# Kernel optimization log

Measured on AMD Instinct MI355X. Metric: run time of the kernel, lower is better.

The kernel has to match this reference:

```python
import jax, jax.numpy as jnp
import numpy as np

N_HEAD = 12

def setup_inputs() -> dict:
    key = jax.random.key(0)
    k1, k2, k3, k4, k5 = jax.random.split(key, 5)
    B, T, C = 2, 2048, 768
    x = jax.random.normal(k1, (B, T, C), dtype=jnp.float32)
    W_attn = jax.random.normal(k2, (C, 3 * C), dtype=jnp.float32) * 0.02
    b_attn = jax.random.normal(k3, (3 * C,), dtype=jnp.float32) * 0.02
    W_proj = jax.random.normal(k4, (C, C), dtype=jnp.float32) * 0.02
    b_proj = jax.random.normal(k5, (C,), dtype=jnp.float32) * 0.02
    return {"x": x, "W_attn": W_attn, "b_attn": b_attn, "W_proj": W_proj, "b_proj": b_proj}

def reference(x, W_attn, b_attn, W_proj, b_proj):
    B, T, C = x.shape
    H = N_HEAD
    hd = C // H
    qkv = x @ W_attn + b_attn  # [B,T,3C]
    q, k, v = jnp.split(qkv, 3, axis=2)
    # [B,H,T,hd]
    q = q.reshape(B, T, H, hd).transpose(0, 2, 1, 3)
    k = k.reshape(B, T, H, hd).transpose(0, 2, 1, 3)
    v = v.reshape(B, T, H, hd).transpose(0, 2, 1, 3)
    att = jnp.einsum('bhqd,bhkd->bhqk', q, k) / jnp.sqrt(jnp.float32(hd))
    causal = jnp.tril(jnp.ones((T, T), dtype=bool))
    att = jnp.where(causal[None, None], att, -jnp.inf)
    att = jax.nn.softmax(att, axis=-1)
    y = jnp.einsum('bhqk,bhkd->bhqd', att, v)  # [B,H,T,hd]
    y = y.transpose(0, 2, 1, 3).reshape(B, T, C)
    return y @ W_proj + b_proj
```

## Files before the change

kernel.cpp:

```cpp
#include <hip/hip_runtime.h>
#include <stdint.h>

typedef unsigned short u16;
typedef __attribute__((ext_vector_type(8))) short bf16x8;
typedef __attribute__((ext_vector_type(4))) float f32x4;

__device__ __forceinline__ u16 f2bf(float f){
  union { float f; uint32_t u; } v; v.f = f;
  uint32_t u = v.u;
  u += 0x7FFFu + ((u >> 16) & 1u);
  return (u16)(u >> 16);
}

__device__ __forceinline__ float fexp2(float x){
#if __has_builtin(__builtin_amdgcn_exp2f)
  return __builtin_amdgcn_exp2f(x);
#else
  return exp2f(x);
#endif
}

__device__ __forceinline__ uint32_t cvtpk_bf16(float lo, float hi){
  uint32_t d;
  asm("v_cvt_pk_bf16_f32 %0, %1, %2" : "=v"(d) : "v"(lo), "v"(hi));
  return d;
}

__device__ __forceinline__ f32x4 mfma_bf16(bf16x8 a, bf16x8 b, f32x4 c){
  return __builtin_amdgcn_mfma_f32_16x16x32_bf16(a, b, c, 0, 0, 0);
}

#define QSCALE 0.1803368801111244f

__global__ __launch_bounds__(256) void cast_x_k(const float* __restrict__ x,
                                                u16* __restrict__ xb, int n4){
  int i = blockIdx.x*256 + threadIdx.x;
  if (i >= n4) return;
  float4 v = reinterpret_cast<const float4*>(x)[i];
  uint2 o;
  o.x = (uint32_t)f2bf(v.x) | ((uint32_t)f2bf(v.y) << 16);
  o.y = (uint32_t)f2bf(v.z) | ((uint32_t)f2bf(v.w) << 16);
  reinterpret_cast<uint2*>(xb)[i] = o;
}

__global__ __launch_bounds__(256) void transpose_cast_k(const float* __restrict__ in,
                                                        u16* __restrict__ out,
                                                        int R, int C){
  __shared__ u16 tile[64][66];
  int c0 = blockIdx.x*64, r0 = blockIdx.y*64;
  int tc = threadIdx.x & 63, t4 = threadIdx.x >> 6;
  #pragma unroll
  for (int i=0;i<16;i++){ int r = t4 + i*4; tile[r][tc] = f2bf(in[(size_t)(r0+r)*C + c0 + tc]); }
  __syncthreads();
  #pragma unroll
  for (int i=0;i<16;i++){ int cc = t4 + i*4; out[(size_t)(c0+cc)*R + r0 + tc] = tile[tc][cc]; }
}

#define LDP 40

__global__ __launch_bounds__(256) void gemm_bf16_k(
    const u16* __restrict__ A, const u16* __restrict__ Bt,
    int M, int N, int K, const float* __restrict__ bias, int mode,
    u16* __restrict__ qo, u16* __restrict__ ko, u16* __restrict__ vo,
    float* __restrict__ fo)
{
  __shared__ u16 As[128*LDP];
  __shared__ u16 Bs[128*LDP];
  const int m0 = blockIdx.y*128, n0 = blockIdx.x*128;
  const int tid = threadIdx.x, lane = tid & 63, wid = tid >> 6;
  const int lr = lane & 15, lg = lane >> 4;
  const int wr = wid >> 1, wc = wid & 1;
  f32x4 acc[4][4] = {};
  const int nk = K >> 5;
  for (int kk = 0; kk < nk; ++kk){
    #pragma unroll
    for (int s = 0; s < 2; ++s){
      int ci = tid + 256*s;
      int row = ci >> 2, ch = ci & 3;
      *(uint4*)&As[row*LDP + ch*8] = *(const uint4*)&A[(size_t)(m0+row)*K + kk*32 + ch*8];
      *(uint4*)&Bs[row*LDP + ch*8] = *(const uint4*)&Bt[(size_t)(n0+row)*K + kk*32 + ch*8];
    }
    __syncthreads();
    bf16x8 af[4], bfr[4];
    #pragma unroll
    for (int m=0;m<4;m++) af[m] = *(const bf16x8*)&As[(wr*64 + m*16 + lr)*LDP + lg*8];
    #pragma unroll
    for (int n=0;n<4;n++) bfr[n] = *(const bf16x8*)&Bs[(wc*64 + n*16 + lr)*LDP + lg*8];
    #pragma unroll
    for (int m=0;m<4;m++)
      #pragma unroll
      for (int n=0;n<4;n++)
        acc[m][n] = mfma_bf16(af[m], bfr[n], acc[m][n]);
    __syncthreads();
  }
  if (mode == 0){
    #pragma unroll
    for (int m=0;m<4;m++)
      #pragma unroll
      for (int n=0;n<4;n++){
        int gn = n0 + wc*64 + n*16 + lr;
        float bv = bias[gn];
        #pragma unroll
        for (int r=0;r<4;r++){
          int gm = m0 + wr*64 + m*16 + lg*4 + r;
          fo[(size_t)gm*N + gn] = acc[m][n][r] + bv;
        }
      }
  } else {
    int which = n0 / 768;
    u16* dst = (which==0) ? qo : ko;
    float sc = (which==0) ? QSCALE : 1.0f;
    #pragma unroll
    for (int m=0;m<4;m++)
      #pragma unroll
      for (int n=0;n<4;n++){
        int gn = n0 + wc*64 + n*16 + lr;
        float bv = bias[gn];
        int cn = gn - which*768;
        int h = cn >> 6, d = cn & 63;
        int gm0 = m0 + wr*64 + m*16 + lg*4;
        int b = gm0 >> 11, t0 = gm0 & 2047;
        if (which < 2){
          #pragma unroll
          for (int r=0;r<4;r++)
            dst[(size_t)((b*12 + h)*2048 + t0 + r)*64 + d] = f2bf((acc[m][n][r] + bv)*sc);
        } else {
          uint2 o;
          o.x = cvtpk_bf16(acc[m][n][0]+bv, acc[m][n][1]+bv);
          o.y = cvtpk_bf16(acc[m][n][2]+bv, acc[m][n][3]+bv);
          *(uint2*)&vo[((size_t)((b*12 + h)*64 + d))*2048 + t0] = o;
        }
      }
  }
}

__global__ __launch_bounds__(256) void attn_k(
    const u16* __restrict__ qp, const u16* __restrict__ kp,
    const u16* __restrict__ vtp, u16* __restrict__ yp)
{
  __shared__ f32x4 ylh[16][64];
  __shared__ float llh[4][16];
  const int i = blockIdx.x;
  const int bh = i % 24;
  const int qb = 63 - (i / 24);
  const int q0 = qb * 32;
  const int q0A = q0, q0B = q0 + 16;
  const int b = bh / 12, h = bh - b*12;
  const size_t base = (size_t)bh * 131072;
  const int tid = threadIdx.x, lane = tid & 63, wid = tid >> 6;
  const int lr = lane & 15, lg = lane >> 4;
  const int qgA = q0A + lr, qgB = q0B + lr;
  const u16* kbase = kp + base;
  const u16* vbase = vtp + base;

  bf16x8 qfA[2], qfB[2];
  #pragma unroll
  for (int kb=0;kb<2;kb++){
    qfA[kb] = *(const bf16x8*)&qp[base + (size_t)qgA*64 + kb*32 + lg*8];
    qfB[kb] = *(const bf16x8*)&qp[base + (size_t)qgB*64 + kb*32 + lg*8];
  }

  f32x4 yA[4] = {}, yB[4] = {};
  float lA = 0.f, lB = 0.f;
  const float m2 = 8.f;
  const int nt = (qb >> 1) + 1;

  uint32_t ko[8], vo[8];
  #pragma unroll
  for (int nb=0;nb<4;nb++){
    int ke = ((nb&1)*32 + (lr>>2)*8 + (nb>>1)*4 + (lr&3))*64 + lg*8;
    ko[nb*2+0] = (uint32_t)(wid*4096 + ke) * 2u;
    ko[nb*2+1] = (uint32_t)(wid*4096 + ke + 32) * 2u;
  }
  #pragma unroll
  for (int n=0;n<4;n++){
    int ve = (n*16+lr)*2048 + lg*8 + wid*64;
    vo[n*2+0] = (uint32_t)ve * 2u;
    vo[n*2+1] = (uint32_t)(ve + 32) * 2u;
  }

  for (int t = wid; t < nt; t += 4){
    bf16x8 kf[8], vf[8];
    #pragma unroll
    for (int j=0;j<8;j++) kf[j] = *(const bf16x8*)((const char*)kbase + ko[j]);
    #pragma unroll
    for (int j=0;j<8;j++) vf[j] = *(const bf16x8*)((const char*)vbase + vo[j]);
    #pragma unroll
    for (int j=0;j<8;j++){ ko[j] += 32768u; vo[j] += 512u; }

    const int k0 = t*64;
    const int nbmin[4] = {0, 32, 4, 36};

    uint32_t pkA[8], pkB[8];
    auto half_qk = [&](int q0H, int qgH, const bf16x8 (&qfH)[2],
                       float &lH, uint32_t (&pkH)[8]){
      f32x4 s[4] = {};
      __builtin_amdgcn_s_setprio(1);
      if (k0      <= q0H + 15){ s[0]=mfma_bf16(kf[0],qfH[0],s[0]); s[0]=mfma_bf16(kf[1],qfH[1],s[0]); }
      if (k0 + 32 <= q0H + 15){ s[1]=mfma_bf16(kf[2],qfH[0],s[1]); s[1]=mfma_bf16(kf[3],qfH[1],s[1]); }
      if (k0 +  4 <= q0H + 15){ s[2]=mfma_bf16(kf[4],qfH[0],s[2]); s[2]=mfma_bf16(kf[5],qfH[1],s[2]); }
      if (k0 + 36 <= q0H + 15){ s[3]=mfma_bf16(kf[6],qfH[0],s[3]); s[3]=mfma_bf16(kf[7],qfH[1],s[3]); }
      __builtin_amdgcn_s_setprio(0);
      if (k0 + 63 > q0H){
        #pragma unroll
        for (int nb=0;nb<4;nb++){
          int kb0 = k0 + (nb&1)*32 + ((nb>>1)&1)*4 + lg*8;
          #pragma unroll
          for (int r=0;r<4;r++)
            if (kb0 + r > qgH) s[nb][r] = -1e30f;
        }
      }
      float lsum = 0.f;
      #pragma unroll
      for (int nb=0;nb<4;nb++){
        if (k0 + nbmin[nb] <= q0H + 15){
          #pragma unroll
          for (int r=0;r<4;r++){
            float p = fexp2(s[nb][r] - m2);
            s[nb][r] = p;
            lsum += p;
          }
        } else {
          #pragma unroll
          for (int r=0;r<4;r++) s[nb][r] = 0.f;
        }
      }
      lH += lsum;
      #pragma unroll
      for (int nb=0;nb<4;nb++){
        pkH[nb*2]   = cvtpk_bf16(s[nb][0], s[nb][1]);
        pkH[nb*2+1] = cvtpk_bf16(s[nb][2], s[nb][3]);
      }
    };
    half_qk(q0A, qgA, qfA, lA, pkA);
    half_qk(q0B, qgB, qfB, lB, pkB);

    __builtin_amdgcn_s_setprio(1);
    {
      union { uint32_t u[4]; bf16x8 v; } pb;
      pb.u[0]=pkA[0]; pb.u[1]=pkA[1]; pb.u[2]=pkA[4]; pb.u[3]=pkA[5];
      yA[0]=mfma_bf16(vf[0],pb.v,yA[0]); yA[1]=mfma_bf16(vf[2],pb.v,yA[1]);
      yA[2]=mfma_bf16(vf[4],pb.v,yA[2]); yA[3]=mfma_bf16(vf[6],pb.v,yA[3]);
      pb.u[0]=pkA[2]; pb.u[1]=pkA[3]; pb.u[2]=pkA[6]; pb.u[3]=pkA[7];
      yA[0]=mfma_bf16(vf[1],pb.v,yA[0]); yA[1]=mfma_bf16(vf[3],pb.v,yA[1]);
      yA[2]=mfma_bf16(vf[5],pb.v,yA[2]); yA[3]=mfma_bf16(vf[7],pb.v,yA[3]);
      pb.u[0]=pkB[0]; pb.u[1]=pkB[1]; pb.u[2]=pkB[4]; pb.u[3]=pkB[5];
      yB[0]=mfma_bf16(vf[0],pb.v,yB[0]); yB[1]=mfma_bf16(vf[2],pb.v,yB[1]);
      yB[2]=mfma_bf16(vf[4],pb.v,yB[2]); yB[3]=mfma_bf16(vf[6],pb.v,yB[3]);
      pb.u[0]=pkB[2]; pb.u[1]=pkB[3]; pb.u[2]=pkB[6]; pb.u[3]=pkB[7];
      yB[0]=mfma_bf16(vf[1],pb.v,yB[0]); yB[1]=mfma_bf16(vf[3],pb.v,yB[1]);
      yB[2]=mfma_bf16(vf[5],pb.v,yB[2]); yB[3]=mfma_bf16(vf[7],pb.v,yB[3]);
    }
    __builtin_amdgcn_s_setprio(0);
  }

  lA += __shfl_xor(lA, 16);  lA += __shfl_xor(lA, 32);
  lB += __shfl_xor(lB, 16);  lB += __shfl_xor(lB, 32);

  #pragma unroll
  for (int hf=0; hf<2; hf++){
    if (hf) __syncthreads();
    #pragma unroll
    for (int n=0;n<4;n++) ylh[wid*4+n][lane] = hf ? yB[n] : yA[n];
    if (lg == 0) llh[wid][lr] = hf ? lB : lA;
    __syncthreads();
    float Ls = (llh[0][lr] + llh[1][lr]) + (llh[2][lr] + llh[3][lr]);
    f32x4 y0 = ylh[0*4+wid][lane], y1 = ylh[1*4+wid][lane],
          y2 = ylh[2*4+wid][lane], y3 = ylh[3*4+wid][lane];
    f32x4 ys;
    #pragma unroll
    for (int r=0;r<4;r++) ys[r] = (y0[r] + y1[r]) + (y2[r] + y3[r]);
    float inv = 1.0f / Ls;
    uint2 o;
    o.x = cvtpk_bf16(ys[0]*inv, ys[1]*inv);
    o.y = cvtpk_bf16(ys[2]*inv, ys[3]*inv);
    *(uint2*)&yp[(size_t)(b*2048 + q0 + hf*16 + lr)*768 + h*64 + wid*16 + lg*4] = o;
  }
}

extern "C" void kernel_launch(void* const* d_in, const int* in_sizes, int n_in,
                              void* d_out, int out_size, void* d_ws, size_t ws_size,
                              hipStream_t stream)
{
  const float* x  = (const float*)d_in[0];
  const float* Wa = (const float*)d_in[1];
  const float* ba = (const float*)d_in[2];
  const float* Wp = (const float*)d_in[3];
  const float* bp = (const float*)d_in[4];
  float* out = (float*)d_out;
  char* ws = (char*)d_ws;
  u16* xb  = (u16*)(ws + 0);
  u16* wt  = (u16*)(ws + 6291456);
  u16* wpt = (u16*)(ws + 9830400);
  u16* qb  = (u16*)(ws + 11010048);
  u16* kb  = (u16*)(ws + 17301504);
  u16* vtb = (u16*)(ws + 23592960);
  u16* yb  = (u16*)(ws + 29884416);

  cast_x_k<<<3072, 256, 0, stream>>>(x, xb, 786432);
  transpose_cast_k<<<dim3(36,12), 256, 0, stream>>>(Wa, wt, 768, 2304);
  transpose_cast_k<<<dim3(12,12), 256, 0, stream>>>(Wp, wpt, 768, 768);
  gemm_bf16_k<<<dim3(18,32), 256, 0, stream>>>(xb, wt, 4096, 2304, 768, ba, 1,
                                               qb, kb, vtb, nullptr);
  attn_k<<<1536, 256, 0, stream>>>(qb, kb, vtb, yb);
  gemm_bf16_k<<<dim3(6,32), 256, 0, stream>>>(yb, wpt, 4096, 768, 768, bp, 0,
                                              nullptr, nullptr, nullptr, out);
}
```

Measured before the change: 126.5 us.

## Halve GEMM M-tile and give each attention block 64 query rows

The GEMM is templated on its number of M fragments and both projections now run with 64-row tiles instead of 128. This doubles the grid and shrinks per-block accumulators, aimed at better CU occupancy and load balance. The attention kernel now handles 64 queries per block, split into four 16-row sub-tiles, so each K/V tile loaded from global memory is reused across twice as many queries and the grid is halved. In exchange, the GEMM reloads each B tile more often, and each attention block does more serial work with more live registers.

```diff
diff --git a/kernel.cpp b/kernel.cpp
--- a/kernel.cpp
+++ b/kernel.cpp
@@ -58,36 +58,43 @@
 
 #define LDP 40
 
+template<int MFRAG>
 __global__ __launch_bounds__(256) void gemm_bf16_k(
     const u16* __restrict__ A, const u16* __restrict__ Bt,
     int M, int N, int K, const float* __restrict__ bias, int mode,
     u16* __restrict__ qo, u16* __restrict__ ko, u16* __restrict__ vo,
     float* __restrict__ fo)
 {
-  __shared__ u16 As[128*LDP];
+  constexpr int BM = MFRAG*32;
+  __shared__ u16 As[BM*LDP];
   __shared__ u16 Bs[128*LDP];
-  const int m0 = blockIdx.y*128, n0 = blockIdx.x*128;
+  const int m0 = blockIdx.y*BM, n0 = blockIdx.x*128;
   const int tid = threadIdx.x, lane = tid & 63, wid = tid >> 6;
   const int lr = lane & 15, lg = lane >> 4;
   const int wr = wid >> 1, wc = wid & 1;
-  f32x4 acc[4][4] = {};
+  f32x4 acc[MFRAG][4] = {};
   const int nk = K >> 5;
   for (int kk = 0; kk < nk; ++kk){
+    #pragma unroll
+    for (int s = 0; s < MFRAG/2; ++s){
+      int ci = tid + 256*s;
+      int row = ci >> 2, ch = ci & 3;
+      *(uint4*)&As[row*LDP + ch*8] = *(const uint4*)&A[(size_t)(m0+row)*K + kk*32 + ch*8];
+    }
     #pragma unroll
     for (int s = 0; s < 2; ++s){
       int ci = tid + 256*s;
       int row = ci >> 2, ch = ci & 3;
-      *(uint4*)&As[row*LDP + ch*8] = *(const uint4*)&A[(size_t)(m0+row)*K + kk*32 + ch*8];
       *(uint4*)&Bs[row*LDP + ch*8] = *(const uint4*)&Bt[(size_t)(n0+row)*K + kk*32 + ch*8];
     }
     __syncthreads();
-    bf16x8 af[4], bfr[4];
-    #pragma unroll
-    for (int m=0;m<4;m++) af[m] = *(const bf16x8*)&As[(wr*64 + m*16 + lr)*LDP + lg*8];
+    bf16x8 af[MFRAG], bfr[4];
+    #pragma unroll
+    for (int m=0;m<MFRAG;m++) af[m] = *(const bf16x8*)&As[(wr*(MFRAG*16) + m*16 + lr)*LDP + lg*8];
     #pragma unroll
     for (int n=0;n<4;n++) bfr[n] = *(const bf16x8*)&Bs[(wc*64 + n*16 + lr)*LDP + lg*8];
     #pragma unroll
-    for (int m=0;m<4;m++)
+    for (int m=0;m<MFRAG;m++)
       #pragma unroll
       for (int n=0;n<4;n++)
         acc[m][n] = mfma_bf16(af[m], bfr[n], acc[m][n]);
@@ -95,14 +102,14 @@
   }
   if (mode == 0){
     #pragma unroll
-    for (int m=0;m<4;m++)
+    for (int m=0;m<MFRAG;m++)
       #pragma unroll
       for (int n=0;n<4;n++){
         int gn = n0 + wc*64 + n*16 + lr;
         float bv = bias[gn];
         #pragma unroll
         for (int r=0;r<4;r++){
-          int gm = m0 + wr*64 + m*16 + lg*4 + r;
+          int gm = m0 + wr*(MFRAG*16) + m*16 + lg*4 + r;
           fo[(size_t)gm*N + gn] = acc[m][n][r] + bv;
         }
       }
@@ -111,14 +118,14 @@
     u16* dst = (which==0) ? qo : ko;
     float sc = (which==0) ? QSCALE : 1.0f;
     #pragma unroll
-    for (int m=0;m<4;m++)
+    for (int m=0;m<MFRAG;m++)
       #pragma unroll
       for (int n=0;n<4;n++){
         int gn = n0 + wc*64 + n*16 + lr;
         float bv = bias[gn];
         int cn = gn - which*768;
         int h = cn >> 6, d = cn & 63;
-        int gm0 = m0 + wr*64 + m*16 + lg*4;
+        int gm0 = m0 + wr*(MFRAG*16) + m*16 + lg*4;
         int b = gm0 >> 11, t0 = gm0 & 2047;
         if (which < 2){
           #pragma unroll
@@ -142,28 +149,28 @@
   __shared__ float llh[4][16];
   const int i = blockIdx.x;
   const int bh = i % 24;
-  const int qb = 63 - (i / 24);
-  const int q0 = qb * 32;
-  const int q0A = q0, q0B = q0 + 16;
+  const int qsb = 31 - (i / 24);
+  const int q0 = qsb * 64;
   const int b = bh / 12, h = bh - b*12;
   const size_t base = (size_t)bh * 131072;
   const int tid = threadIdx.x, lane = tid & 63, wid = tid >> 6;
   const int lr = lane & 15, lg = lane >> 4;
-  const int qgA = q0A + lr, qgB = q0B + lr;
   const u16* kbase = kp + base;
   const u16* vbase = vtp + base;
 
-  bf16x8 qfA[2], qfB[2];
+  bf16x8 qf0[2], qf1[2], qf2[2], qf3[2];
   #pragma unroll
   for (int kb=0;kb<2;kb++){
-    qfA[kb] = *(const bf16x8*)&qp[base + (size_t)qgA*64 + kb*32 + lg*8];
-    qfB[kb] = *(const bf16x8*)&qp[base + (size_t)qgB*64 + kb*32 + lg*8];
-  }
-
-  f32x4 yA[4] = {}, yB[4] = {};
-  float lA = 0.f, lB = 0.f;
+    qf0[kb] = *(const bf16x8*)&qp[base + (size_t)(q0      + lr)*64 + kb*32 + lg*8];
+    qf1[kb] = *(const bf16x8*)&qp[base + (size_t)(q0 + 16 + lr)*64 + kb*32 + lg*8];
+    qf2[kb] = *(const bf16x8*)&qp[base + (size_t)(q0 + 32 + lr)*64 + kb*32 + lg*8];
+    qf3[kb] = *(const bf16x8*)&qp[base + (size_t)(q0 + 48 + lr)*64 + kb*32 + lg*8];
+  }
+
+  f32x4 y0[4] = {}, y1[4] = {}, y2[4] = {}, y3[4] = {};
+  float l0 = 0.f, l1 = 0.f, l2 = 0.f, l3 = 0.f;
   const float m2 = 8.f;
-  const int nt = (qb >> 1) + 1;
+  const int nt = qsb + 1;
 
   uint32_t ko[8], vo[8];
   #pragma unroll
@@ -191,9 +198,8 @@
     const int k0 = t*64;
     const int nbmin[4] = {0, 32, 4, 36};
 
-    uint32_t pkA[8], pkB[8];
-    auto half_qk = [&](int q0H, int qgH, const bf16x8 (&qfH)[2],
-                       float &lH, uint32_t (&pkH)[8]){
+    auto do_half = [&](int q0H, const bf16x8 (&qfH)[2], f32x4 (&yH)[4], float &lH){
+      const int qgH = q0H + lr;
       f32x4 s[4] = {};
       __builtin_amdgcn_s_setprio(1);
       if (k0      <= q0H + 15){ s[0]=mfma_bf16(kf[0],qfH[0],s[0]); s[0]=mfma_bf16(kf[1],qfH[1],s[0]); }
@@ -226,56 +232,55 @@
         }
       }
       lH += lsum;
+      uint32_t pk[8];
       #pragma unroll
       for (int nb=0;nb<4;nb++){
-        pkH[nb*2]   = cvtpk_bf16(s[nb][0], s[nb][1]);
-        pkH[nb*2+1] = cvtpk_bf16(s[nb][2], s[nb][3]);
-      }
+        pk[nb*2]   = cvtpk_bf16(s[nb][0], s[nb][1]);
+        pk[nb*2+1] = cvtpk_bf16(s[nb][2], s[nb][3]);
+      }
+      __builtin_amdgcn_s_setprio(1);
+      union { uint32_t u[4]; bf16x8 v; } pb;
+      pb.u[0]=pk[0]; pb.u[1]=pk[1]; pb.u[2]=pk[4]; pb.u[3]=pk[5];
+      yH[0]=mfma_bf16(vf[0],pb.v,yH[0]); yH[1]=mfma_bf16(vf[2],pb.v,yH[1]);
+      yH[2]=mfma_bf16(vf[4],pb.v,yH[2]); yH[3]=mfma_bf16(vf[6],pb.v,yH[3]);
+      pb.u[0]=pk[2]; pb.u[1]=pk[3]; pb.u[2]=pk[6]; pb.u[3]=pk[7];
+      yH[0]=mfma_bf16(vf[1],pb.v,yH[0]); yH[1]=mfma_bf16(vf[3],pb.v,yH[1]);
+      yH[2]=mfma_bf16(vf[5],pb.v,yH[2]); yH[3]=mfma_bf16(vf[7],pb.v,yH[3]);
+      __builtin_amdgcn_s_setprio(0);
     };
-    half_qk(q0A, qgA, qfA, lA, pkA);
-    half_qk(q0B, qgB, qfB, lB, pkB);
-
-    __builtin_amdgcn_s_setprio(1);
-    {
-      union { uint32_t u[4]; bf16x8 v; } pb;
-      pb.u[0]=pkA[0]; pb.u[1]=pkA[1]; pb.u[2]=pkA[4]; pb.u[3]=pkA[5];
-      yA[0]=mfma_bf16(vf[0],pb.v,yA[0]); yA[1]=mfma_bf16(vf[2],pb.v,yA[1]);
-      yA[2]=mfma_bf16(vf[4],pb.v,yA[2]); yA[3]=mfma_bf16(vf[6],pb.v,yA[3]);
-      pb.u[0]=pkA[2]; pb.u[1]=pkA[3]; pb.u[2]=pkA[6]; pb.u[3]=pkA[7];
-      yA[0]=mfma_bf16(vf[1],pb.v,yA[0]); yA[1]=mfma_bf16(vf[3],pb.v,yA[1]);
-      yA[2]=mfma_bf16(vf[5],pb.v,yA[2]); yA[3]=mfma_bf16(vf[7],pb.v,yA[3]);
-      pb.u[0]=pkB[0]; pb.u[1]=pkB[1]; pb.u[2]=pkB[4]; pb.u[3]=pkB[5];
-      yB[0]=mfma_bf16(vf[0],pb.v,yB[0]); yB[1]=mfma_bf16(vf[2],pb.v,yB[1]);
-      yB[2]=mfma_bf16(vf[4],pb.v,yB[2]); yB[3]=mfma_bf16(vf[6],pb.v,yB[3]);
-      pb.u[0]=pkB[2]; pb.u[1]=pkB[3]; pb.u[2]=pkB[6]; pb.u[3]=pkB[7];
-      yB[0]=mfma_bf16(vf[1],pb.v,yB[0]); yB[1]=mfma_bf16(vf[3],pb.v,yB[1]);
-      yB[2]=mfma_bf16(vf[5],pb.v,yB[2]); yB[3]=mfma_bf16(vf[7],pb.v,yB[3]);
-    }
-    __builtin_amdgcn_s_setprio(0);
-  }
-
-  lA += __shfl_xor(lA, 16);  lA += __shfl_xor(lA, 32);
-  lB += __shfl_xor(lB, 16);  lB += __shfl_xor(lB, 32);
-
-  #pragma unroll
-  for (int hf=0; hf<2; hf++){
+    do_half(q0     , qf0, y0, l0);
+    do_half(q0 + 16, qf1, y1, l1);
+    do_half(q0 + 32, qf2, y2, l2);
+    do_half(q0 + 48, qf3, y3, l3);
+  }
+
+  l0 += __shfl_xor(l0, 16);  l0 += __shfl_xor(l0, 32);
+  l1 += __shfl_xor(l1, 16);  l1 += __shfl_xor(l1, 32);
+  l2 += __shfl_xor(l2, 16);  l2 += __shfl_xor(l2, 32);
+  l3 += __shfl_xor(l3, 16);  l3 += __shfl_xor(l3, 32);
+
+  auto phase = [&](const f32x4 (&yH)[4], float lH, int hf){
     if (hf) __syncthreads();
     #pragma unroll
-    for (int n=0;n<4;n++) ylh[wid*4+n][lane] = hf ? yB[n] : yA[n];
-    if (lg == 0) llh[wid][lr] = hf ? lB : lA;
+    for (int n=0;n<4;n++) ylh[wid*4+n][lane] = yH[n];
+    if (lg == 0) llh[wid][lr] = lH;
     __syncthreads();
     float Ls = (llh[0][lr] + llh[1][lr]) + (llh[2][lr] + llh[3][lr]);
-    f32x4 y0 = ylh[0*4+wid][lane], y1 = ylh[1*4+wid][lane],
-          y2 = ylh[2*4+wid][lane], y3 = ylh[3*4+wid][lane];
+    f32x4 a0 = ylh[0*4+wid][lane], a1 = ylh[1*4+wid][lane],
+          a2 = ylh[2*4+wid][lane], a3 = ylh[3*4+wid][lane];
     f32x4 ys;
     #pragma unroll
-    for (int r=0;r<4;r++) ys[r] = (y0[r] + y1[r]) + (y2[r] + y3[r]);
+    for (int r=0;r<4;r++) ys[r] = (a0[r] + a1[r]) + (a2[r] + a3[r]);
     float inv = 1.0f / Ls;
     uint2 o;
     o.x = cvtpk_bf16(ys[0]*inv, ys[1]*inv);
     o.y = cvtpk_bf16(ys[2]*inv, ys[3]*inv);
     *(uint2*)&yp[(size_t)(b*2048 + q0 + hf*16 + lr)*768 + h*64 + wid*16 + lg*4] = o;
-  }
+  };
+  phase(y0, l0, 0);
+  phase(y1, l1, 1);
+  phase(y2, l2, 2);
+  phase(y3, l3, 3);
 }
 
 extern "C" void kernel_launch(void* const* d_in, const int* in_sizes, int n_in,
@@ -300,9 +305,9 @@
   cast_x_k<<<3072, 256, 0, stream>>>(x, xb, 786432);
   transpose_cast_k<<<dim3(36,12), 256, 0, stream>>>(Wa, wt, 768, 2304);
   transpose_cast_k<<<dim3(12,12), 256, 0, stream>>>(Wp, wpt, 768, 768);
-  gemm_bf16_k<<<dim3(18,32), 256, 0, stream>>>(xb, wt, 4096, 2304, 768, ba, 1,
-                                               qb, kb, vtb, nullptr);
-  attn_k<<<1536, 256, 0, stream>>>(qb, kb, vtb, yb);
-  gemm_bf16_k<<<dim3(6,32), 256, 0, stream>>>(yb, wpt, 4096, 768, 768, bp, 0,
-                                              nullptr, nullptr, nullptr, out);
-}
+  gemm_bf16_k<2><<<dim3(18,64), 256, 0, stream>>>(xb, wt, 4096, 2304, 768, ba, 1,
+                                                  qb, kb, vtb, nullptr);
+  attn_k<<<768, 256, 0, stream>>>(qb, kb, vtb, yb);
+  gemm_bf16_k<2><<<dim3(6,64), 256, 0, stream>>>(yb, wpt, 4096, 768, 768, bp, 0,
+                                                 nullptr, nullptr, nullptr, out);
+}
```

Measured after the change: 121.9 us, median of 2. 3.6% less time.
